# Kernel optimization log

Measured on AMD Instinct MI355X. Metric: run time of the kernel, lower is better.

The kernel has to match this reference:

```python
import jax, jax.numpy as jnp
import numpy as np

B, T, D = 64, 512, 512
K_CODES = 256
K_FUTURE = 2


def _gru(x, w_ih, w_hh, b_ih, b_hh):
    # x: [B,T,D]; PyTorch GRU gate order: r, z, n; weights [3D, D]
    xg = jnp.einsum('btd,gd->btg', x, w_ih) + b_ih  # [B,T,3D] precomputed input gates

    def step(h, xg_t):
        hg = h @ w_hh.T + b_hh                      # [B,3D]
        xr, xz, xn = jnp.split(xg_t, 3, axis=-1)
        hr, hz, hn = jnp.split(hg, 3, axis=-1)
        r = jax.nn.sigmoid(xr + hr)
        z = jax.nn.sigmoid(xz + hz)
        n = jnp.tanh(xn + r * hn)
        h_new = (1.0 - z) * n + z * h
        return h_new, h_new

    h0 = jnp.zeros((x.shape[0], w_hh.shape[1]), x.dtype)
    _, hs = jax.lax.scan(step, h0, jnp.swapaxes(xg, 0, 1))
    return jnp.swapaxes(hs, 0, 1)  # [B,T,D]


def setup_inputs() -> dict:
    key = jax.random.key(0)
    ks = jax.random.split(key, 8)
    return {
        'features': jax.random.normal(ks[0], (B, T, D), jnp.float32),
        'codebook': jax.random.uniform(ks[1], (K_CODES, D), jnp.float32, -0.1, 0.1),
        'w_ih': jax.random.normal(ks[2], (3 * D, D), jnp.float32) * 0.02,
        'w_hh': jax.random.normal(ks[3], (3 * D, D), jnp.float32) * 0.02,
        'b_ih': jax.random.normal(ks[4], (3 * D,), jnp.float32) * 0.02,
        'b_hh': jax.random.normal(ks[5], (3 * D,), jnp.float32) * 0.02,
        'proj_w': jax.random.normal(ks[6], (D, D), jnp.float32) * 0.02,
        'proj_b': jax.random.normal(ks[7], (D,), jnp.float32) * 0.02,
    }


def reference(features, codebook, w_ih, w_hh, b_ih, b_hh, proj_w, proj_b):
    b, t, d = features.shape
    # --- quantize: cdist + argmin + gather (squared dists give same argmin) ---
    flat = features.reshape(-1, d)                              # [B*T, D]
    d2 = (jnp.sum(flat * flat, axis=1, keepdims=True)
          - 2.0 * flat @ codebook.T
          + jnp.sum(codebook * codebook, axis=1))               # [B*T, K]
    indices = jnp.argmin(d2, axis=1)                            # [B*T]
    quantized = codebook[indices].reshape(b, t, d)              # gather
    indices = indices.reshape(b, t)

    # --- context prediction loss ---
    hidden = _gru(quantized, w_ih, w_hh, b_ih, b_hh)            # [B,T,D]
    context_proj = hidden @ proj_w.T + proj_b                   # [B,T,D]
    k_max = min(K_FUTURE, t - 1)
    cp_loss = jnp.float32(0.0)
    for k in range(1, k_max + 1):
        cp_loss = cp_loss + jnp.mean((context_proj[:, :-k] - features[:, k:]) ** 2)
    cp_loss = cp_loss / k_max

    # --- VQ loss (stop_gradient mirrors torch .detach()) ---
    commitment_loss = jnp.mean((jax.lax.stop_gradient(features) - quantized) ** 2)
    codebook_loss = jnp.mean((features - jax.lax.stop_gradient(quantized)) ** 2)
    vq_loss = commitment_loss + 0.25 * codebook_loss

    total_loss = cp_loss + vq_loss
    return quantized, indices, total_loss, cp_loss, vq_loss
```

## Files before the change

### kernel.cpp

```cpp
#include <hip/hip_runtime.h>
#include <hip/hip_bf16.h>

#define B_ 64
#define T_ 512
#define D_ 512
#define K_ 256
#define G3 1536

typedef __attribute__((ext_vector_type(8))) short sh8;
typedef __attribute__((ext_vector_type(4))) short sh4;
typedef __attribute__((ext_vector_type(4))) float fx4;
typedef __attribute__((ext_vector_type(4))) int   ix4;

__device__ __forceinline__ short f2bf(float x) {
  __hip_bfloat16 h = __float2bfloat16(x);
  union { __hip_bfloat16 h; short s; } u; u.h = h; return u.s;
}
__device__ __forceinline__ float sigm(float x) { return 1.f / (1.f + __expf(-x)); }

__global__ void k_cnorm(const float* __restrict__ cb, double* __restrict__ cn) {
  int c = threadIdx.x;
  if (c < K_) {
    double s = 0.0;
    for (int k = 0; k < D_; ++k) { double v = cb[c * D_ + k]; s += v * v; }
    cn[c] = s;
  }
}

__global__ __launch_bounds__(256) void k_cg(const float* __restrict__ cb,
                                            const float* __restrict__ wih,
                                            const float* __restrict__ bih,
                                            float* __restrict__ cg) {
  __shared__ float wl[16][512];
  int j0 = blockIdx.x * 16, c0 = blockIdx.y * 64;
  for (int v = threadIdx.x; v < 16 * 128; v += 256) {
    int r = v >> 7, q = v & 127;
    *(fx4*)&wl[r][q * 4] = *(const fx4*)&wih[(j0 + r) * D_ + q * 4];
  }
  __syncthreads();
  for (int p = threadIdx.x; p < 1024; p += 256) {
    int j = p >> 6, c = c0 + (p & 63);
    fx4 a = {0.f, 0.f, 0.f, 0.f};
    const float* cbr = &cb[c * D_];
    for (int q = 0; q < 128; ++q) {
      fx4 w4 = *(fx4*)&wl[j][q * 4];
      fx4 c4 = *(const fx4*)&cbr[q * 4];
      a += w4 * c4;
    }
    cg[c * G3 + j0 + j] = ((a.x + a.y) + (a.z + a.w)) + bih[j0 + j];
  }
}

__global__ void k_cvt(const float* __restrict__ src, __hip_bfloat16* __restrict__ dst, int n4) {
  int i = blockIdx.x * blockDim.x + threadIdx.x;
  if (i < n4) {
    fx4 v = *(const fx4*)&src[i * 4];
    sh4 o; o[0] = f2bf(v.x); o[1] = f2bf(v.y); o[2] = f2bf(v.z); o[3] = f2bf(v.w);
    *(sh4*)&dst[i * 4] = o;
  }
}

__global__ __launch_bounds__(256) void k_quant(const float* __restrict__ feat,
                                               const float* __restrict__ cb,
                                               const double* __restrict__ cn,
                                               int* __restrict__ idxw,
                                               float* __restrict__ outq,
                                               float* __restrict__ outi,
                                               double* __restrict__ lacc) {
  __shared__ float fl[16][516];
  __shared__ double ss1[16][16], ss2[16][16];
  __shared__ int ii1[16][16], ii2[16][16];
  __shared__ int idxl[16];
  __shared__ float rsv[4];
  int row0 = blockIdx.x * 16;
  int tid = threadIdx.x;
  for (int v = tid; v < 16 * 128; v += 256) {
    int r = v >> 7, q = v & 127;
    *(fx4*)&fl[r][q * 4] = *(const fx4*)&feat[(row0 + r) * D_ + q * 4];
  }
  __syncthreads();
  int r = tid & 15, g = tid >> 4;
  fx4 acc[16];
#pragma unroll
  for (int c = 0; c < 16; ++c) acc[c] = (fx4){0.f, 0.f, 0.f, 0.f};
  for (int ch = 0; ch < 8; ++ch) {
    fx4 fc[16];
#pragma unroll
    for (int q = 0; q < 16; ++q) fc[q] = *(fx4*)&fl[r][ch * 64 + q * 4];
#pragma unroll
    for (int c = 0; c < 16; ++c) {
      const float* cbp = &cb[(g * 16 + c) * D_ + ch * 64];
#pragma unroll
      for (int q = 0; q < 16; ++q) {
        fx4 c4 = *(const fx4*)&cbp[q * 4];
        acc[c] += fc[q] * c4;
      }
    }
  }
  double b1 = 1e300, b2 = 1e300; int i1 = 0, i2 = 0;
#pragma unroll
  for (int c = 0; c < 16; ++c) {
    int ci = g * 16 + c;
    double dot = (double)acc[c].x + acc[c].y + acc[c].z + acc[c].w;
    double s = cn[ci] - 2.0 * dot;
    if (s < b1) { b2 = b1; i2 = i1; b1 = s; i1 = ci; }
    else if (s < b2) { b2 = s; i2 = ci; }
  }
  ss1[r][g] = b1; ss2[r][g] = b2; ii1[r][g] = i1; ii2[r][g] = i2;
  __syncthreads();
  if (tid < 16) {
    int rr = tid;
    double c1 = 1e300, c2 = 1e300; int j1 = 0, j2 = 0;
    for (int g2 = 0; g2 < 16; ++g2) {
      double s = ss1[rr][g2]; int ix = ii1[rr][g2];
      if (s < c1 || (s == c1 && ix < j1)) { c2 = c1; j2 = j1; c1 = s; j1 = ix; }
      else if (s < c2 || (s == c2 && ix < j2)) { c2 = s; j2 = ix; }
      s = ss2[rr][g2]; ix = ii2[rr][g2];
      if (s < c1 || (s == c1 && ix < j1)) { c2 = c1; j2 = j1; c1 = s; j1 = ix; }
      else if (s < c2 || (s == c2 && ix < j2)) { c2 = s; j2 = ix; }
    }
    int pick = j1;
    if (c2 - c1 < 1e-4) {
      double d1 = 0.0, d2 = 0.0;
      for (int k = 0; k < D_; ++k) {
        double fv = fl[rr][k];
        d1 += fv * (double)cb[j1 * D_ + k];
        d2 += fv * (double)cb[j2 * D_ + k];
      }
      double e1 = cn[j1] - 2.0 * d1, e2 = cn[j2] - 2.0 * d2;
      if (e2 < e1 || (e2 == e1 && j2 < j1)) pick = j2;
    }
    idxl[rr] = pick;
    idxw[row0 + rr] = pick;
    outi[row0 + rr] = (float)pick;
  }
  __syncthreads();
  float vs = 0.f;
  for (int v = tid; v < 16 * 128; v += 256) {
    int rr = v >> 7, q = v & 127;
    fx4 c4 = *(const fx4*)&cb[idxl[rr] * D_ + q * 4];
    *(fx4*)&outq[(row0 + rr) * D_ + q * 4] = c4;
    fx4 f4 = *(fx4*)&fl[rr][q * 4];
    fx4 d = f4 - c4;
    vs += d.x * d.x + d.y * d.y + d.z * d.z + d.w * d.w;
  }
#pragma unroll
  for (int off = 32; off > 0; off >>= 1) vs += __shfl_down(vs, off);
  if ((tid & 63) == 0) rsv[tid >> 6] = vs;
  __syncthreads();
  if (tid == 0) atomicAdd(&lacc[2], (double)(rsv[0] + rsv[1] + rsv[2] + rsv[3]));
}

__global__ __launch_bounds__(256, 1) void k_gru(const float* __restrict__ whh,
                                                const float* __restrict__ bhh,
                                                const float* __restrict__ cg,
                                                const int* __restrict__ idx,
                                                __hip_bfloat16* __restrict__ hid,
                                                unsigned int* __restrict__ flag,
                                                int* __restrict__ xcca,
                                                unsigned int* __restrict__ bar0) {
  int bid = blockIdx.x;
  int g = bid & 7, s = bid >> 3;
  int tid = threadIdx.x;
  int w = tid >> 6, lane = tid & 63, l15 = lane & 15, l4 = lane >> 4;

  sh8 A0[16], A1[16], A2[16];
#pragma unroll
  for (int kt = 0; kt < 16; ++kt) {
#pragma unroll
    for (int t3 = 0; t3 < 3; ++t3) {
      int lr = 48 * w + 16 * t3 + l15;
      int gate = lr >> 6, din = lr & 63;
      const float* wr = &whh[(gate * 512 + s * 64 + din) * D_];
      int k0 = kt * 32 + l4 * 8;
      fx4 x = *(const fx4*)&wr[k0];
      fx4 y = *(const fx4*)&wr[k0 + 4];
      sh8 t;
      t[0] = f2bf(x.x); t[1] = f2bf(x.y); t[2] = f2bf(x.z); t[3] = f2bf(x.w);
      t[4] = f2bf(y.x); t[5] = f2bf(y.y); t[6] = f2bf(y.z); t[7] = f2bf(y.w);
      if (t3 == 0) A0[kt] = t; else if (t3 == 1) A1[kt] = t; else A2[kt] = t;
    }
  }

  __shared__ float hl[8][64];
  __shared__ float hg[192][9];
  __shared__ int ixs[8];
  __shared__ int sh_fast;
  for (int i = tid; i < 512; i += 256) ((float*)hl)[i] = 0.f;

  if (tid == 0) {
    int xcc = 0;
    asm volatile("s_getreg_b32 %0, hwreg(HW_REG_XCC_ID)" : "=s"(xcc));
    __hip_atomic_store(&xcca[bid], xcc, __ATOMIC_RELEASE, __HIP_MEMORY_SCOPE_AGENT);
    __hip_atomic_fetch_add(bar0, 1u, __ATOMIC_ACQ_REL, __HIP_MEMORY_SCOPE_AGENT);
    while (__hip_atomic_load(bar0, __ATOMIC_ACQUIRE, __HIP_MEMORY_SCOPE_AGENT) < 64u)
      __builtin_amdgcn_s_sleep(2);
    int x0 = __hip_atomic_load(&xcca[g], __ATOMIC_RELAXED, __HIP_MEMORY_SCOPE_AGENT);
    int f = 1;
    for (int m = 1; m < 8; ++m)
      if (__hip_atomic_load(&xcca[g + 8 * m], __ATOMIC_RELAXED, __HIP_MEMORY_SCOPE_AGENT) != x0)
        f = 0;
    sh_fast = f;
  }
  __syncthreads();
  const bool fast = (sh_fast != 0);

  for (int t = 0; t < T_; ++t) {
    if (tid < 8) ixs[tid] = idx[(g * 8 + tid) * T_ + t];

    fx4 a0 = {0, 0, 0, 0}, a1 = {0, 0, 0, 0}, a2 = {0, 0, 0, 0};
    if (t > 0) {
      if (tid < 8) {
        while (__hip_atomic_load(&flag[tid * 8 + g], __ATOMIC_RELAXED,
                                 __HIP_MEMORY_SCOPE_AGENT) < (unsigned)t)
          __builtin_amdgcn_s_sleep(1);
      }
      if (!fast && tid == 0) __threadfence();
      __syncthreads();

      const __hip_bfloat16* hrow =
          &hid[((size_t)(g * 8 + (l15 & 7)) * T_ + (t - 1)) * D_];
#pragma unroll
      for (int kt = 0; kt < 16; ++kt) {
        sh8 bfr = {0, 0, 0, 0, 0, 0, 0, 0};
        if (l15 < 8) bfr = *(const sh8*)&hrow[kt * 32 + l4 * 8];
        a0 = __builtin_amdgcn_mfma_f32_16x16x32_bf16(A0[kt], bfr, a0, 0, 0, 0);
        a1 = __builtin_amdgcn_mfma_f32_16x16x32_bf16(A1[kt], bfr, a1, 0, 0, 0);
        a2 = __builtin_amdgcn_mfma_f32_16x16x32_bf16(A2[kt], bfr, a2, 0, 0, 0);
      }
    }
    if (l15 < 8) {
#pragma unroll
      for (int rg = 0; rg < 4; ++rg) {
        hg[48 * w +      l4 * 4 + rg][l15] = a0[rg];
        hg[48 * w + 16 + l4 * 4 + rg][l15] = a1[rg];
        hg[48 * w + 32 + l4 * 4 + rg][l15] = a2[rg];
      }
    }
    __syncthreads();
#pragma unroll
    for (int ii = 0; ii < 2; ++ii) {
      int i = tid + ii * 256;
      int b = i >> 6, d = i & 63;
      int ci = ixs[b];
      const float* cgr = &cg[ci * G3 + s * 64 + d];
      int dg = s * 64 + d;
      float hr = hg[d][b]       + bhh[dg];
      float hz = hg[64 + d][b]  + bhh[512 + dg];
      float hn = hg[128 + d][b] + bhh[1024 + dg];
      float rr = sigm(cgr[0] + hr);
      float zz = sigm(cgr[512] + hz);
      float nn = tanhf(cgr[1024] + rr * hn);
      float hp = hl[b][d];
      float hv = (1.f - zz) * nn + zz * hp;
      hl[b][d] = hv;
      hid[((size_t)(g * 8 + b) * T_ + t) * D_ + dg] = __float2bfloat16(hv);
    }
    __syncthreads();
    if (tid == 0) {
      if (!fast) __threadfence();
      __hip_atomic_store(&flag[bid], (unsigned)(t + 1), __ATOMIC_RELAXED,
                         __HIP_MEMORY_SCOPE_AGENT);
    }
  }
}

__global__ __launch_bounds__(256) void k_proj(const __hip_bfloat16* __restrict__ hid,
                                              const __hip_bfloat16* __restrict__ pwb,
                                              const float* __restrict__ pb,
                                              const float* __restrict__ feat,
                                              double* __restrict__ lacc) {
  __shared__ char Bl[512 * 64];
  __shared__ char Al[32 * 64];
  __shared__ float rs1[4], rs2[4];
  int Mb = blockIdx.x * 32;
  int tid = threadIdx.x;
  int w = tid >> 6, lane = tid & 63, l15 = lane & 15, l4 = lane >> 4;
  fx4 acc[2][8];
#pragma unroll
  for (int a = 0; a < 2; ++a)
#pragma unroll
    for (int b = 0; b < 8; ++b) acc[a][b] = (fx4){0, 0, 0, 0};

  for (int kc = 0; kc < 16; ++kc) {
    for (int v = tid; v < 2048; v += 256) {
      int rw = v >> 2, sg = v & 3;
      ix4 d = *(const ix4*)&pwb[rw * D_ + kc * 32 + sg * 8];
      *(ix4*)(Bl + rw * 64 + ((sg * 16) ^ ((rw & 7) << 4))) = d;
    }
    if (tid < 128) {
      int rw = tid >> 2, sg = tid & 3;
      ix4 d = *(const ix4*)&hid[(size_t)(Mb + rw) * D_ + kc * 32 + sg * 8];
      *(ix4*)(Al + rw * 64 + ((sg * 16) ^ ((rw & 7) << 4))) = d;
    }
    __syncthreads();
    sh8 af0, af1;
    {
      int m = l15;
      af0 = *(const sh8*)(Al + m * 64 + ((l4 * 16) ^ ((m & 7) << 4)));
      m = 16 + l15;
      af1 = *(const sh8*)(Al + m * 64 + ((l4 * 16) ^ ((m & 7) << 4)));
    }
#pragma unroll
    for (int nt = 0; nt < 8; ++nt) {
      int n = (w * 8 + nt) * 16 + l15;
      sh8 bf = *(const sh8*)(Bl + n * 64 + ((l4 * 16) ^ ((n & 7) << 4)));
      acc[0][nt] = __builtin_amdgcn_mfma_f32_16x16x32_bf16(af0, bf, acc[0][nt], 0, 0, 0);
      acc[1][nt] = __builtin_amdgcn_mfma_f32_16x16x32_bf16(af1, bf, acc[1][nt], 0, 0, 0);
    }
    __syncthreads();
  }

  float s1 = 0.f, s2 = 0.f;
#pragma unroll
  for (int mt = 0; mt < 2; ++mt) {
#pragma unroll
    for (int nt = 0; nt < 8; ++nt) {
      int n = (w * 8 + nt) * 16 + l15;
      float bias = pb[n];
#pragma unroll
      for (int rg = 0; rg < 4; ++rg) {
        int m = Mb + mt * 16 + l4 * 4 + rg;
        float val = acc[mt][nt][rg] + bias;
        int t = m & (T_ - 1);
        if (t < T_ - 1) { float d = val - feat[(size_t)(m + 1) * D_ + n]; s1 += d * d; }
        if (t < T_ - 2) { float d = val - feat[(size_t)(m + 2) * D_ + n]; s2 += d * d; }
      }
    }
  }
#pragma unroll
  for (int off = 32; off > 0; off >>= 1) {
    s1 += __shfl_down(s1, off);
    s2 += __shfl_down(s2, off);
  }
  if (lane == 0) { rs1[w] = s1; rs2[w] = s2; }
  __syncthreads();
  if (tid == 0) {
    atomicAdd(&lacc[0], (double)rs1[0] + rs1[1] + rs1[2] + rs1[3]);
    atomicAdd(&lacc[1], (double)rs2[0] + rs2[1] + rs2[2] + rs2[3]);
  }
}

__global__ void k_fin(const double* __restrict__ lacc, float* __restrict__ outl) {
  if (threadIdx.x == 0) {
    double cp = 0.5 * (lacc[0] / ((double)B_ * (T_ - 1) * D_) +
                       lacc[1] / ((double)B_ * (T_ - 2) * D_));
    double vq = 1.25 * lacc[2] / ((double)B_ * T_ * D_);
    outl[0] = (float)(cp + vq);
    outl[1] = (float)cp;
    outl[2] = (float)vq;
  }
}

extern "C" void kernel_launch(void* const* d_in, const int* in_sizes, int n_in,
                              void* d_out, int out_size, void* d_ws, size_t ws_size,
                              hipStream_t stream) {
  (void)in_sizes; (void)n_in; (void)out_size; (void)ws_size;
  const float* feat = (const float*)d_in[0];
  const float* cb   = (const float*)d_in[1];
  const float* wih  = (const float*)d_in[2];
  const float* whh  = (const float*)d_in[3];
  const float* bih  = (const float*)d_in[4];
  const float* bhh  = (const float*)d_in[5];
  const float* pw   = (const float*)d_in[6];
  const float* pb   = (const float*)d_in[7];

  float* out  = (float*)d_out;
  float* outq = out;
  float* outi = out + (size_t)B_ * T_ * D_;
  float* outl = outi + B_ * T_;

  char* ws = (char*)d_ws;
  size_t o = 0;
  auto alloc = [&](size_t sz) { void* p = ws + o; o += (sz + 255) & ~(size_t)255; return p; };
  float*          cg   = (float*)alloc(sizeof(float) * K_ * G3);
  double*         cn   = (double*)alloc(sizeof(double) * K_);
  int*            idxw = (int*)alloc(sizeof(int) * B_ * T_);
  __hip_bfloat16* pwb  = (__hip_bfloat16*)alloc(sizeof(__hip_bfloat16) * D_ * D_);
  double*         lacc = (double*)alloc(sizeof(double) * 4);
  unsigned*       flag = (unsigned*)alloc(sizeof(unsigned) * 64);
  int*            xcca = (int*)alloc(sizeof(int) * 64);
  unsigned*       bar0 = (unsigned*)alloc(sizeof(unsigned) * 4);
  __hip_bfloat16* hid  = (__hip_bfloat16*)alloc(sizeof(__hip_bfloat16) * (size_t)B_ * T_ * D_);

  hipMemsetAsync(lacc, 0, sizeof(double) * 4, stream);
  hipMemsetAsync(flag, 0, sizeof(unsigned) * 64, stream);
  hipMemsetAsync(xcca, 0, sizeof(int) * 64, stream);
  hipMemsetAsync(bar0, 0, sizeof(unsigned) * 4, stream);

  hipLaunchKernelGGL(k_cnorm, dim3(1), dim3(256), 0, stream, cb, cn);
  hipLaunchKernelGGL(k_cg, dim3(96, 4), dim3(256), 0, stream, cb, wih, bih, cg);
  hipLaunchKernelGGL(k_cvt, dim3(256), dim3(256), 0, stream, pw, pwb, D_ * D_ / 4);
  hipLaunchKernelGGL(k_quant, dim3(2048), dim3(256), 0, stream, feat, cb, cn, idxw, outq, outi, lacc);
  hipLaunchKernelGGL(k_gru, dim3(64), dim3(256), 0, stream, whh, bhh, cg, idxw, hid, flag, xcca, bar0);
  hipLaunchKernelGGL(k_proj, dim3(1024), dim3(256), 0, stream, hid, pwb, pb, feat, lacc);
  hipLaunchKernelGGL(k_fin, dim3(1), dim3(64), 0, stream, lacc, outl);
}
```

Before: 2.947 ms.

## Compute GRU gate update in MFMA registers, fold biases, pad sync flags

Each GRU block's weight rows are now remapped so every lane's MFMA accumulator holds the r, z and n gate values for the same four hidden units. This lets the gate nonlinearity and state update run directly in registers and removes the shared-memory transpose and one __syncthreads per timestep. The r/z recurrent biases are folded into the precomputed codebook-gate table, and tanh uses an exp-based formula. Per-block progress flags are padded to separate cache lines and the spin loop drops its sleep. The trade-off is more register pressure, idle lanes during the update step, and busier spinning.

```diff
diff --git a/kernel.cpp b/kernel.cpp
--- a/kernel.cpp
+++ b/kernel.cpp
@@ -17,6 +17,10 @@
   union { __hip_bfloat16 h; short s; } u; u.h = h; return u.s;
 }
 __device__ __forceinline__ float sigm(float x) { return 1.f / (1.f + __expf(-x)); }
+__device__ __forceinline__ float tanh_fast(float x) {
+  float e2 = __expf(-2.f * x);
+  return (1.f - e2) / (1.f + e2);
+}
 
 __global__ void k_cnorm(const float* __restrict__ cb, double* __restrict__ cn) {
   int c = threadIdx.x;
@@ -30,6 +34,7 @@
 __global__ __launch_bounds__(256) void k_cg(const float* __restrict__ cb,
                                             const float* __restrict__ wih,
                                             const float* __restrict__ bih,
+                                            const float* __restrict__ bhh,
                                             float* __restrict__ cg) {
   __shared__ float wl[16][512];
   int j0 = blockIdx.x * 16, c0 = blockIdx.y * 64;
@@ -47,7 +52,9 @@
       fx4 c4 = *(const fx4*)&cbr[q * 4];
       a += w4 * c4;
     }
-    cg[c * G3 + j0 + j] = ((a.x + a.y) + (a.z + a.w)) + bih[j0 + j];
+    int jg = j0 + j;
+    float bias = bih[jg] + (jg < 1024 ? bhh[jg] : 0.f);
+    cg[c * G3 + jg] = ((a.x + a.y) + (a.z + a.w)) + bias;
   }
 }
 
@@ -169,25 +176,25 @@
   for (int kt = 0; kt < 16; ++kt) {
 #pragma unroll
     for (int t3 = 0; t3 < 3; ++t3) {
-      int lr = 48 * w + 16 * t3 + l15;
-      int gate = lr >> 6, din = lr & 63;
-      const float* wr = &whh[(gate * 512 + s * 64 + din) * D_];
+      const float* wr = &whh[((t3 * 512) + s * 64 + w * 16 + l15) * D_];
       int k0 = kt * 32 + l4 * 8;
       fx4 x = *(const fx4*)&wr[k0];
       fx4 y = *(const fx4*)&wr[k0 + 4];
-      sh8 t;
-      t[0] = f2bf(x.x); t[1] = f2bf(x.y); t[2] = f2bf(x.z); t[3] = f2bf(x.w);
-      t[4] = f2bf(y.x); t[5] = f2bf(y.y); t[6] = f2bf(y.z); t[7] = f2bf(y.w);
-      if (t3 == 0) A0[kt] = t; else if (t3 == 1) A1[kt] = t; else A2[kt] = t;
-    }
-  }
-
-  __shared__ float hl[8][64];
-  __shared__ float hg[192][9];
-  __shared__ int ixs[8];
+      sh8 tt;
+      tt[0] = f2bf(x.x); tt[1] = f2bf(x.y); tt[2] = f2bf(x.z); tt[3] = f2bf(x.w);
+      tt[4] = f2bf(y.x); tt[5] = f2bf(y.y); tt[6] = f2bf(y.z); tt[7] = f2bf(y.w);
+      if (t3 == 0) A0[kt] = tt; else if (t3 == 1) A1[kt] = tt; else A2[kt] = tt;
+    }
+  }
+
+  const bool act = (l15 < 8);
+  const int b = l15;
+  const int dg0 = s * 64 + w * 16 + l4 * 4;
+
+  fx4 bn = *(const fx4*)&bhh[1024 + dg0];
+  fx4 hp = {0.f, 0.f, 0.f, 0.f};
+
   __shared__ int sh_fast;
-  for (int i = tid; i < 512; i += 256) ((float*)hl)[i] = 0.f;
-
   if (tid == 0) {
     int xcc = 0;
     asm volatile("s_getreg_b32 %0, hwreg(HW_REG_XCC_ID)" : "=s"(xcc));
@@ -201,19 +208,27 @@
       if (__hip_atomic_load(&xcca[g + 8 * m], __ATOMIC_RELAXED, __HIP_MEMORY_SCOPE_AGENT) != x0)
         f = 0;
     sh_fast = f;
+    __threadfence();
   }
   __syncthreads();
   const bool fast = (sh_fast != 0);
 
   for (int t = 0; t < T_; ++t) {
-    if (tid < 8) ixs[tid] = idx[(g * 8 + tid) * T_ + t];
+    fx4 cr = {0, 0, 0, 0}, cz = {0, 0, 0, 0}, cnn = {0, 0, 0, 0};
+    if (act) {
+      int ci = idx[(g * 8 + b) * T_ + t];
+      const float* cgr = &cg[(size_t)ci * G3 + dg0];
+      cr  = *(const fx4*)cgr;
+      cz  = *(const fx4*)(cgr + 512);
+      cnn = *(const fx4*)(cgr + 1024);
+    }
 
     fx4 a0 = {0, 0, 0, 0}, a1 = {0, 0, 0, 0}, a2 = {0, 0, 0, 0};
     if (t > 0) {
       if (tid < 8) {
-        while (__hip_atomic_load(&flag[tid * 8 + g], __ATOMIC_RELAXED,
-                                 __HIP_MEMORY_SCOPE_AGENT) < (unsigned)t)
-          __builtin_amdgcn_s_sleep(1);
+        const unsigned* fp = &flag[(tid * 8 + g) * 32];
+        while (__hip_atomic_load(fp, __ATOMIC_RELAXED, __HIP_MEMORY_SCOPE_AGENT)
+               < (unsigned)t) {}
       }
       if (!fast && tid == 0) __threadfence();
       __syncthreads();
@@ -223,43 +238,30 @@
 #pragma unroll
       for (int kt = 0; kt < 16; ++kt) {
         sh8 bfr = {0, 0, 0, 0, 0, 0, 0, 0};
-        if (l15 < 8) bfr = *(const sh8*)&hrow[kt * 32 + l4 * 8];
+        if (act) bfr = *(const sh8*)&hrow[kt * 32 + l4 * 8];
         a0 = __builtin_amdgcn_mfma_f32_16x16x32_bf16(A0[kt], bfr, a0, 0, 0, 0);
         a1 = __builtin_amdgcn_mfma_f32_16x16x32_bf16(A1[kt], bfr, a1, 0, 0, 0);
         a2 = __builtin_amdgcn_mfma_f32_16x16x32_bf16(A2[kt], bfr, a2, 0, 0, 0);
       }
     }
-    if (l15 < 8) {
+
+    if (act) {
+      sh4 hb4;
 #pragma unroll
       for (int rg = 0; rg < 4; ++rg) {
-        hg[48 * w +      l4 * 4 + rg][l15] = a0[rg];
-        hg[48 * w + 16 + l4 * 4 + rg][l15] = a1[rg];
-        hg[48 * w + 32 + l4 * 4 + rg][l15] = a2[rg];
-      }
-    }
-    __syncthreads();
-#pragma unroll
-    for (int ii = 0; ii < 2; ++ii) {
-      int i = tid + ii * 256;
-      int b = i >> 6, d = i & 63;
-      int ci = ixs[b];
-      const float* cgr = &cg[ci * G3 + s * 64 + d];
-      int dg = s * 64 + d;
-      float hr = hg[d][b]       + bhh[dg];
-      float hz = hg[64 + d][b]  + bhh[512 + dg];
-      float hn = hg[128 + d][b] + bhh[1024 + dg];
-      float rr = sigm(cgr[0] + hr);
-      float zz = sigm(cgr[512] + hz);
-      float nn = tanhf(cgr[1024] + rr * hn);
-      float hp = hl[b][d];
-      float hv = (1.f - zz) * nn + zz * hp;
-      hl[b][d] = hv;
-      hid[((size_t)(g * 8 + b) * T_ + t) * D_ + dg] = __float2bfloat16(hv);
+        float rr = sigm(cr[rg] + a0[rg]);
+        float zz = sigm(cz[rg] + a1[rg]);
+        float nn = tanh_fast(cnn[rg] + rr * (a2[rg] + bn[rg]));
+        float hv = (1.f - zz) * nn + zz * hp[rg];
+        hp[rg] = hv;
+        hb4[rg] = f2bf(hv);
+      }
+      *(sh4*)&hid[((size_t)(g * 8 + b) * T_ + t) * D_ + dg0] = hb4;
     }
     __syncthreads();
     if (tid == 0) {
       if (!fast) __threadfence();
-      __hip_atomic_store(&flag[bid], (unsigned)(t + 1), __ATOMIC_RELAXED,
+      __hip_atomic_store(&flag[bid * 32], (unsigned)(t + 1), __ATOMIC_RELAXED,
                          __HIP_MEMORY_SCOPE_AGENT);
     }
   }
@@ -378,18 +380,18 @@
   int*            idxw = (int*)alloc(sizeof(int) * B_ * T_);
   __hip_bfloat16* pwb  = (__hip_bfloat16*)alloc(sizeof(__hip_bfloat16) * D_ * D_);
   double*         lacc = (double*)alloc(sizeof(double) * 4);
-  unsigned*       flag = (unsigned*)alloc(sizeof(unsigned) * 64);
+  unsigned*       flag = (unsigned*)alloc(sizeof(unsigned) * 64 * 32);
   int*            xcca = (int*)alloc(sizeof(int) * 64);
   unsigned*       bar0 = (unsigned*)alloc(sizeof(unsigned) * 4);
   __hip_bfloat16* hid  = (__hip_bfloat16*)alloc(sizeof(__hip_bfloat16) * (size_t)B_ * T_ * D_);
 
   hipMemsetAsync(lacc, 0, sizeof(double) * 4, stream);
-  hipMemsetAsync(flag, 0, sizeof(unsigned) * 64, stream);
+  hipMemsetAsync(flag, 0, sizeof(unsigned) * 64 * 32, stream);
   hipMemsetAsync(xcca, 0, sizeof(int) * 64, stream);
   hipMemsetAsync(bar0, 0, sizeof(unsigned) * 4, stream);
 
   hipLaunchKernelGGL(k_cnorm, dim3(1), dim3(256), 0, stream, cb, cn);
-  hipLaunchKernelGGL(k_cg, dim3(96, 4), dim3(256), 0, stream, cb, wih, bih, cg);
+  hipLaunchKernelGGL(k_cg, dim3(96, 4), dim3(256), 0, stream, cb, wih, bih, bhh, cg);
   hipLaunchKernelGGL(k_cvt, dim3(256), dim3(256), 0, stream, pw, pwb, D_ * D_ / 4);
   hipLaunchKernelGGL(k_quant, dim3(2048), dim3(256), 0, stream, feat, cb, cn, idxw, outq, outi, lacc);
   hipLaunchKernelGGL(k_gru, dim3(64), dim3(256), 0, stream, whh, bhh, cg, idxw, hid, flag, xcca, bar0);
```

Result: slower. 3.223 ms (+9.4%).
